# Optimization experiments

Measured on AMD Instinct MI355X. Metric: run time of the kernel, lower is better.

Reference implementation:

```python
import jax, jax.numpy as jnp
import numpy as np

N = 100000   # nodes
E = 1600000  # edges
B = 64       # graphs
F = 16       # node features
H = 128      # hidden dim
G = 8        # graph features
C = 2        # classes
NGIN = 2     # extra GIN layers after the first
BN_EPS = 1e-5


def elu01(x):
    # F.elu with alpha=0.1
    return jnp.where(x > 0, x, 0.1 * jnp.expm1(x))


def batchnorm(h, gamma, beta):
    # training-mode BatchNorm1d: biased batch statistics
    mu = h.mean(axis=0)
    var = h.var(axis=0)
    return (h - mu) * jax.lax.rsqrt(var + BN_EPS) * gamma + beta


def gin_layer(x, src, dst, W1, b1, gm, bt, W2, b2):
    # GINConv eps=0: MLP(x + sum_{j->i} x_j), then ELU(0.1)
    agg = jax.ops.segment_sum(x[src], dst, num_segments=x.shape[0])
    h = (x + agg) @ W1 + b1
    h = jax.nn.relu(batchnorm(h, gm, bt))
    return elu01(h @ W2 + b2)


def setup_inputs() -> dict:
    key = jax.random.key(0)
    ks = jax.random.split(key, 24)
    s = 0.05
    inp = {
        "h0": jax.random.normal(ks[0], (N, F), jnp.float32),
        "coord0": jax.random.normal(ks[1], (N, 3), jnp.float32),
        "g0": jax.random.normal(ks[2], (B, G), jnp.float32),
        "edge_index": jax.random.randint(ks[3], (2, E), 0, N, jnp.int32),
        "batch": jnp.sort(jax.random.randint(ks[4], (N,), 0, B, jnp.int32)),
        # first GIN layer: (F+3) -> H -> H
        "w1_0": jax.random.normal(ks[5], (F + 3, H), jnp.float32) * s,
        "b1_0": jnp.zeros((H,), jnp.float32),
        "gm_0": jnp.ones((H,), jnp.float32),
        "bt_0": jnp.zeros((H,), jnp.float32),
        "w2_0": jax.random.normal(ks[6], (H, H), jnp.float32) * s,
        "b2_0": jnp.zeros((H,), jnp.float32),
        # NGIN stacked layers: H -> H -> H
        "w1_r": jax.random.normal(ks[7], (NGIN, H, H), jnp.float32) * s,
        "b1_r": jnp.zeros((NGIN, H), jnp.float32),
        "gm_r": jnp.ones((NGIN, H), jnp.float32),
        "bt_r": jnp.zeros((NGIN, H), jnp.float32),
        "w2_r": jax.random.normal(ks[8], (NGIN, H, H), jnp.float32) * s,
        "b2_r": jnp.zeros((NGIN, H), jnp.float32),
        # classifier: (2H+G) -> H -> C
        "cw1": jax.random.normal(ks[9], (2 * H + G, H), jnp.float32) * s,
        "cb1": jnp.zeros((H,), jnp.float32),
        "cgm": jnp.ones((H,), jnp.float32),
        "cbt": jnp.zeros((H,), jnp.float32),
        "cw2": jax.random.normal(ks[10], (H, C), jnp.float32) * s,
        "cb2": jnp.zeros((C,), jnp.float32),
    }
    return inp


def reference(h0, coord0, g0, edge_index, batch,
              w1_0, b1_0, gm_0, bt_0, w2_0, b2_0,
              w1_r, b1_r, gm_r, bt_r, w2_r, b2_r,
              cw1, cb1, cgm, cbt, cw2, cb2):
    src, dst = edge_index[0], edge_index[1]
    x = jnp.concatenate([h0, coord0], axis=1)  # [N, F+3]
    x = gin_layer(x, src, dst, w1_0, b1_0, gm_0, bt_0, w2_0, b2_0)
    for i in range(NGIN):
        x = gin_layer(x, src, dst, w1_r[i], b1_r[i], gm_r[i], bt_r[i], w2_r[i], b2_r[i])
    # global mean + max pooling per graph
    nb = g0.shape[0]
    cnt = jax.ops.segment_sum(jnp.ones((x.shape[0], 1), x.dtype), batch, num_segments=nb)
    mean_p = jax.ops.segment_sum(x, batch, num_segments=nb) / jnp.maximum(cnt, 1.0)
    max_p = jax.ops.segment_max(x, batch, num_segments=nb)
    pooled = jnp.concatenate([mean_p, max_p], axis=-1)  # [B, 2H]
    z = jnp.concatenate([pooled, g0], axis=1)           # [B, 2H+G]
    z = elu01(z @ cw1 + cb1)
    z = batchnorm(z, cgm, cbt)
    logits = z @ cw2 + cb2
    return jax.nn.softmax(logits, axis=1)
```

## Files before the change

kernel.cpp:

```cpp
#include <hip/hip_runtime.h>
#include <math.h>

#define NN 100000
#define EE 1600000
#define BB 64
#define FF 16
#define HH 128
#define GG 8
#define K0 19
#define BN_EPS 1e-5f
#define PCH 16
#define BSHIFT 8
#define BNODES 256
#define NBINS 391
#define BCAP 8192
#define ACH 2048
#define NB_WP 320
#define NB_X0 12500
#define STSLOT 8

typedef short bf16x8 __attribute__((ext_vector_type(8)));
typedef float f32x4 __attribute__((ext_vector_type(4)));

__device__ __forceinline__ float elu01f(float v) {
    return v > 0.f ? v : 0.1f * (__expf(v) - 1.f);
}

__device__ __forceinline__ unsigned f2bfu(float f) {
    unsigned u = __float_as_uint(f);
    unsigned r = u + 0x7FFFu + ((u >> 16) & 1u);
    return r >> 16;
}
__device__ __forceinline__ short f2bf(float f) { return (short)f2bfu(f); }
__device__ __forceinline__ float bfu2f(unsigned short b) {
    return __uint_as_float(((unsigned)b) << 16);
}
__device__ __forceinline__ float bflo(unsigned u) { return __uint_as_float(u << 16); }
__device__ __forceinline__ float bfhi(unsigned u) { return __uint_as_float(u & 0xffff0000u); }

__global__ __launch_bounds__(256) void k_binA(const int* __restrict__ esrc, const int* __restrict__ edst,
                                              int* __restrict__ bincnt, uint2* __restrict__ binbuf) {
    __shared__ int hist[NBINS];
    __shared__ int gbase[NBINS];
    __shared__ int cur[NBINS];
    __shared__ int sc[512];
    __shared__ uint2 ebuf[ACH];
    __shared__ uint2 sorted[ACH];
    int tid = threadIdx.x;
    int e0 = blockIdx.x * ACH;
    int n = min(ACH, EE - e0);
    for (int i = tid; i < NBINS; i += 256) hist[i] = 0;
    __syncthreads();
    for (int i = tid; i < n; i += 256) {
        int s = esrc[e0 + i];
        int d = edst[e0 + i];
        ebuf[i] = make_uint2((unsigned)s, (unsigned)d);
        atomicAdd(&hist[d >> BSHIFT], 1);
    }
    __syncthreads();
    sc[tid] = (tid < NBINS) ? hist[tid] : 0;
    sc[tid + 256] = (tid + 256 < NBINS) ? hist[tid + 256] : 0;
    __syncthreads();
    for (int off = 1; off < 512; off <<= 1) {
        int a0 = sc[tid], a1 = sc[tid + 256];
        int b0 = (tid >= off) ? sc[tid - off] : 0;
        int b1 = (tid + 256 >= off) ? sc[tid + 256 - off] : 0;
        __syncthreads();
        sc[tid] = a0 + b0;
        sc[tid + 256] = a1 + b1;
        __syncthreads();
    }
    for (int b = tid; b < NBINS; b += 256) {
        int c = hist[b];
        gbase[b] = (c > 0) ? atomicAdd(&bincnt[b], c) : 0;
        cur[b] = (b > 0) ? sc[b - 1] : 0;
    }
    __syncthreads();
    for (int i = tid; i < n; i += 256) {
        uint2 e = ebuf[i];
        int b = (int)(e.y >> BSHIFT);
        int pos = atomicAdd(&cur[b], 1);
        sorted[pos] = e;
    }
    __syncthreads();
    for (int i = tid; i < n; i += 256) {
        uint2 e = sorted[i];
        int b = (int)(e.y >> BSHIFT);
        int ls = (b > 0) ? sc[b - 1] : 0;
        int gpos = gbase[b] + (i - ls);
        binbuf[(size_t)b * BCAP + gpos] = e;
    }
}

__global__ void k_binscan(const int* __restrict__ bincnt, int* __restrict__ binstart, int* __restrict__ rp,
                          const int* __restrict__ batch, int* __restrict__ gptr) {
    __shared__ int sc[512];
    int t = threadIdx.x;
    sc[t] = (t < NBINS) ? bincnt[t] : 0;
    __syncthreads();
    for (int off = 1; off < 512; off <<= 1) {
        int v = (t >= off) ? sc[t - off] : 0;
        __syncthreads();
        sc[t] += v;
        __syncthreads();
    }
    if (t < NBINS) binstart[t] = (t > 0) ? sc[t - 1] : 0;
    if (t == 0) rp[NN] = EE;
    if (t <= BB) {
        int lo = 0, hi = NN;
        while (lo < hi) { int mid = (lo + hi) >> 1; if (batch[mid] < t) lo = mid + 1; else hi = mid; }
        gptr[t] = lo;
    }
}

__global__ __launch_bounds__(256) void k_binB(const uint2* __restrict__ binbuf, const int* __restrict__ bincnt,
                                              const int* __restrict__ binstart,
                                              int* __restrict__ rp, int* __restrict__ srcs) {
    __shared__ int hist[BNODES];
    __shared__ int scx[BNODES];
    __shared__ int scur[BNODES];
    __shared__ int sbuf[BCAP];
    int b = blockIdx.x;
    int n = bincnt[b];
    int tid = threadIdx.x;
    hist[tid] = 0;
    __syncthreads();
    const uint2* eb = binbuf + (size_t)b * BCAP;
    for (int i = tid; i < n; i += 256)
        atomicAdd(&hist[eb[i].y & (BNODES - 1)], 1);
    __syncthreads();
    scx[tid] = hist[tid];
    __syncthreads();
    for (int off = 1; off < 256; off <<= 1) {
        int v = (tid >= off) ? scx[tid - off] : 0;
        __syncthreads();
        scx[tid] += v;
        __syncthreads();
    }
    int base = binstart[b];
    int excl = (tid > 0) ? scx[tid - 1] : 0;
    int node = (b << BSHIFT) + tid;
    if (node < NN) rp[node] = base + excl;
    scur[tid] = excl;
    __syncthreads();
    for (int i = tid; i < n; i += 256) {
        uint2 e = eb[i];
        int pos = atomicAdd(&scur[e.y & (BNODES - 1)], 1);
        sbuf[pos] = (int)e.x;
    }
    __syncthreads();
    for (int i = tid; i < n; i += 256) srcs[base + i] = sbuf[i];
}

__global__ __launch_bounds__(256) void k_prep(const float* __restrict__ w2_0, const float* __restrict__ w1_r,
                                              const float* __restrict__ w2_r, short* __restrict__ wt,
                                              const float* __restrict__ h0, const float* __restrict__ coord,
                                              unsigned short* __restrict__ x0) {
    int b = blockIdx.x;
    if (b < NB_WP) {
        int t = b * 256 + threadIdx.x;
        if (t >= 5 * HH * HH) return;
        int m = t >> 14;
        int rem = t & 16383;
        int col = rem >> 7;
        int k = rem & 127;
        const float* src = (m == 0) ? w2_0 : (m <= 2 ? w1_r + (size_t)(m - 1) * HH * HH
                                                     : w2_r + (size_t)(m - 3) * HH * HH);
        wt[t] = f2bf(src[k * HH + col]);
    } else {
        int i = (b - NB_WP) * 256 + threadIdx.x;
        if (i >= NN * 32) return;
        int node = i >> 5, k = i & 31;
        float v = 0.f;
        if (k < FF) v = h0[node * FF + k];
        else if (k < K0) v = coord[node * 3 + (k - FF)];
        x0[i] = (unsigned short)f2bfu(v);
    }
}

template<int K>
__global__ __launch_bounds__(256) void k_l0(const uint4* __restrict__ x4, const int* __restrict__ rp,
        const int* __restrict__ srcs, const float* __restrict__ W, const float* __restrict__ bias,
        unsigned short* __restrict__ out, float* __restrict__ gstat) {
    constexpr int SK = ((K + 3) / 4) * 4 + 4;
    __shared__ __align__(16) float yt[32 * SK];
    __shared__ float red[256];
    int tid = threadIdx.x;
    int row0 = blockIdx.x * 32;
    int wave = tid >> 6, lane = tid & 63;
    int e = lane >> 2, q = lane & 3;
    for (int rr = 0; rr < 8; ++rr) {
        int r = (wave << 3) + rr;
        int grow = row0 + r;
        float acc[8];
        if (e == 0) {
            uint4 u = x4[(size_t)grow * 4 + q];
            acc[0] = bflo(u.x); acc[1] = bfhi(u.x);
            acc[2] = bflo(u.y); acc[3] = bfhi(u.y);
            acc[4] = bflo(u.z); acc[5] = bfhi(u.z);
            acc[6] = bflo(u.w); acc[7] = bfhi(u.w);
        } else {
            #pragma unroll
            for (int j = 0; j < 8; j++) acc[j] = 0.f;
        }
        int beg = rp[grow], end = rp[grow + 1];
        for (int p = beg; p < end; p += 16) {
            bool act = e < (end - p);
            int sn = act ? srcs[p + e] : 0;
            uint4 u = x4[(size_t)sn * 4 + q];
            float m = act ? 1.f : 0.f;
            acc[0] = fmaf(m, bflo(u.x), acc[0]); acc[1] = fmaf(m, bfhi(u.x), acc[1]);
            acc[2] = fmaf(m, bflo(u.y), acc[2]); acc[3] = fmaf(m, bfhi(u.y), acc[3]);
            acc[4] = fmaf(m, bflo(u.z), acc[4]); acc[5] = fmaf(m, bfhi(u.z), acc[5]);
            acc[6] = fmaf(m, bflo(u.w), acc[6]); acc[7] = fmaf(m, bfhi(u.w), acc[7]);
        }
        #pragma unroll
        for (int mask = 4; mask <= 32; mask <<= 1)
            #pragma unroll
            for (int j = 0; j < 8; j++) acc[j] += __shfl_xor(acc[j], mask, 64);
        if (e == 0 && q < 3) {
            #pragma unroll
            for (int j = 0; j < 8; j++) yt[r * SK + q * 8 + j] = acc[j];
        }
    }
    __syncthreads();
    int col = tid & 127;
    int rg = tid >> 7;
    float facc[16];
    #pragma unroll
    for (int r = 0; r < 16; r++) facc[r] = 0.f;
    const float* ybase = &yt[rg * 16 * SK];
    int kk = 0;
    for (; kk + 4 <= K; kk += 4) {
        float w0 = W[(kk + 0) * HH + col];
        float w1 = W[(kk + 1) * HH + col];
        float w2 = W[(kk + 2) * HH + col];
        float w3 = W[(kk + 3) * HH + col];
        #pragma unroll
        for (int r = 0; r < 16; r++) {
            const float4 v = *(const float4*)&ybase[r * SK + kk];
            facc[r] = fmaf(v.x, w0, facc[r]);
            facc[r] = fmaf(v.y, w1, facc[r]);
            facc[r] = fmaf(v.z, w2, facc[r]);
            facc[r] = fmaf(v.w, w3, facc[r]);
        }
    }
    if constexpr (K % 4 != 0) {
        float w[4];
        #pragma unroll
        for (int j = 0; j < 4; j++) w[j] = (kk + j < K) ? W[(kk + j) * HH + col] : 0.f;
        #pragma unroll
        for (int r = 0; r < 16; r++) {
            const float4 v = *(const float4*)&ybase[r * SK + kk];
            facc[r] = fmaf(v.x, w[0], facc[r]);
            facc[r] = fmaf(v.y, w[1], facc[r]);
            facc[r] = fmaf(v.z, w[2], facc[r]);
            facc[r] = fmaf(v.w, w[3], facc[r]);
        }
    }
    float bcol = bias[col];
    float s = 0.f, s2 = 0.f;
    #pragma unroll
    for (int r = 0; r < 16; r++) {
        float hv = facc[r] + bcol;
        out[(size_t)(row0 + rg * 16 + r) * HH + col] = (unsigned short)f2bfu(hv);
        s += hv; s2 = fmaf(hv, hv, s2);
    }
    int sl = (blockIdx.x & (STSLOT - 1)) << 8;
    red[tid] = s; __syncthreads();
    if (tid < 128) atomicAdd(&gstat[sl + tid], s + red[tid + 128]);
    __syncthreads();
    red[tid] = s2; __syncthreads();
    if (tid < 128) atomicAdd(&gstat[sl + 128 + tid], s2 + red[tid + 128]);
}

__global__ __launch_bounds__(256) void k_agg128_bf(const unsigned* __restrict__ x, const int* __restrict__ rp,
                                                   const int* __restrict__ srcs, unsigned* __restrict__ y) {
    int w = (blockIdx.x * 256 + threadIdx.x) >> 6;
    int lane = threadIdx.x & 63;
    if (w >= NN) return;
    int beg = rp[w], end = rp[w + 1];
    unsigned us = x[(size_t)w * 64 + lane];
    float ax = bflo(us), ay = bfhi(us);
    float bx = 0.f, by = 0.f;
    float cx = 0.f, cy = 0.f;
    float dx = 0.f, dy = 0.f;
    int p = beg;
    for (; p + 16 <= end; p += 16) {
        int s0 = srcs[p + 0], s1 = srcs[p + 1], s2 = srcs[p + 2], s3 = srcs[p + 3];
        int s4 = srcs[p + 4], s5 = srcs[p + 5], s6 = srcs[p + 6], s7 = srcs[p + 7];
        int s8 = srcs[p + 8], s9 = srcs[p + 9], sa = srcs[p + 10], sb = srcs[p + 11];
        int sc_ = srcs[p + 12], sd = srcs[p + 13], se = srcs[p + 14], sf = srcs[p + 15];
        unsigned u0 = x[(size_t)s0 * 64 + lane];
        unsigned u1 = x[(size_t)s1 * 64 + lane];
        unsigned u2 = x[(size_t)s2 * 64 + lane];
        unsigned u3 = x[(size_t)s3 * 64 + lane];
        unsigned u4 = x[(size_t)s4 * 64 + lane];
        unsigned u5 = x[(size_t)s5 * 64 + lane];
        unsigned u6 = x[(size_t)s6 * 64 + lane];
        unsigned u7 = x[(size_t)s7 * 64 + lane];
        unsigned u8 = x[(size_t)s8 * 64 + lane];
        unsigned u9 = x[(size_t)s9 * 64 + lane];
        unsigned ua = x[(size_t)sa * 64 + lane];
        unsigned ub = x[(size_t)sb * 64 + lane];
        unsigned uc = x[(size_t)sc_ * 64 + lane];
        unsigned ud = x[(size_t)sd * 64 + lane];
        unsigned ue = x[(size_t)se * 64 + lane];
        unsigned uf = x[(size_t)sf * 64 + lane];
        ax += (bflo(u0) + bflo(u1)) + (bflo(u2) + bflo(u3));
        ay += (bfhi(u0) + bfhi(u1)) + (bfhi(u2) + bfhi(u3));
        bx += (bflo(u4) + bflo(u5)) + (bflo(u6) + bflo(u7));
        by += (bfhi(u4) + bfhi(u5)) + (bfhi(u6) + bfhi(u7));
        cx += (bflo(u8) + bflo(u9)) + (bflo(ua) + bflo(ub));
        cy += (bfhi(u8) + bfhi(u9)) + (bfhi(ua) + bfhi(ub));
        dx += (bflo(uc) + bflo(ud)) + (bflo(ue) + bflo(uf));
        dy += (bfhi(uc) + bfhi(ud)) + (bfhi(ue) + bfhi(uf));
    }
    for (; p + 8 <= end; p += 8) {
        int s0 = srcs[p + 0], s1 = srcs[p + 1], s2 = srcs[p + 2], s3 = srcs[p + 3];
        int s4 = srcs[p + 4], s5 = srcs[p + 5], s6 = srcs[p + 6], s7 = srcs[p + 7];
        unsigned u0 = x[(size_t)s0 * 64 + lane];
        unsigned u1 = x[(size_t)s1 * 64 + lane];
        unsigned u2 = x[(size_t)s2 * 64 + lane];
        unsigned u3 = x[(size_t)s3 * 64 + lane];
        unsigned u4 = x[(size_t)s4 * 64 + lane];
        unsigned u5 = x[(size_t)s5 * 64 + lane];
        unsigned u6 = x[(size_t)s6 * 64 + lane];
        unsigned u7 = x[(size_t)s7 * 64 + lane];
        ax += (bflo(u0) + bflo(u1)) + (bflo(u2) + bflo(u3));
        ay += (bfhi(u0) + bfhi(u1)) + (bfhi(u2) + bfhi(u3));
        bx += (bflo(u4) + bflo(u5)) + (bflo(u6) + bflo(u7));
        by += (bfhi(u4) + bfhi(u5)) + (bfhi(u6) + bfhi(u7));
    }
    for (; p < end; ++p) {
        unsigned u = x[(size_t)srcs[p] * 64 + lane];
        ax += bflo(u);
        ay += bfhi(u);
    }
    ax += bx + cx + dx;
    ay += by + cy + dy;
    y[(size_t)w * 64 + lane] = f2bfu(ax) | (f2bfu(ay) << 16);
}

__global__ __launch_bounds__(256) void k_gemm_s1(const unsigned short* __restrict__ in,
        const short* __restrict__ WT, const float* __restrict__ bias,
        unsigned short* __restrict__ out, float* __restrict__ gstat) {
    __shared__ __align__(16) short Al[64 * 136];
    __shared__ float lsum[HH], lsq[HH];
    int tid = threadIdx.x;
    if (tid < HH) { lsum[tid] = 0.f; lsq[tid] = 0.f; }
    int row0 = blockIdx.x * 64;
    {
        int r = tid >> 2;
        int k0 = (tid & 3) * 32;
        int grow = row0 + r;
        uint4* d4 = (uint4*)&Al[r * 136 + k0];
        if (grow < NN) {
            const uint4* s4 = (const uint4*)(in + (size_t)grow * HH + k0);
            d4[0] = s4[0]; d4[1] = s4[1]; d4[2] = s4[2]; d4[3] = s4[3];
        } else {
            uint4 z = {0, 0, 0, 0};
            d4[0] = z; d4[1] = z; d4[2] = z; d4[3] = z;
        }
    }
    __syncthreads();
    int wave = tid >> 6;
    int lane = tid & 63;
    int ln = lane & 15, quad = lane >> 4;
    int wcol0 = wave * 32;
    f32x4 acc[4][2];
    #pragma unroll
    for (int rt = 0; rt < 4; rt++)
        #pragma unroll
        for (int ct = 0; ct < 2; ct++) acc[rt][ct] = (f32x4){0.f, 0.f, 0.f, 0.f};
    #pragma unroll
    for (int ks = 0; ks < 4; ks++) {
        bf16x8 a[4], b[2];
        #pragma unroll
        for (int ct = 0; ct < 2; ct++)
            b[ct] = *(const bf16x8*)(WT + (size_t)(wcol0 + ct * 16 + ln) * HH + ks * 32 + quad * 8);
        #pragma unroll
        for (int rt = 0; rt < 4; rt++)
            a[rt] = *(const bf16x8*)(&Al[(rt * 16 + ln) * 136 + ks * 32 + quad * 8]);
        #pragma unroll
        for (int rt = 0; rt < 4; rt++)
            #pragma unroll
            for (int ct = 0; ct < 2; ct++)
                acc[rt][ct] = __builtin_amdgcn_mfma_f32_16x16x32_bf16(a[rt], b[ct], acc[rt][ct], 0, 0, 0);
    }
    float b0 = bias[wcol0 + ln];
    float b1 = bias[wcol0 + 16 + ln];
    float s[2] = {0.f, 0.f}, s2[2] = {0.f, 0.f};
    #pragma unroll
    for (int rt = 0; rt < 4; rt++) {
        #pragma unroll
        for (int r = 0; r < 4; r++) {
            int grow = row0 + rt * 16 + quad * 4 + r;
            if (grow < NN) {
                float hv0 = acc[rt][0][r] + b0;
                float hv1 = acc[rt][1][r] + b1;
                out[(size_t)grow * HH + wcol0 + ln] = (unsigned short)f2bfu(hv0);
                out[(size_t)grow * HH + wcol0 + 16 + ln] = (unsigned short)f2bfu(hv1);
                s[0] += hv0; s2[0] = fmaf(hv0, hv0, s2[0]);
                s[1] += hv1; s2[1] = fmaf(hv1, hv1, s2[1]);
            }
        }
    }
    atomicAdd(&lsum[wcol0 + ln], s[0]);
    atomicAdd(&lsum[wcol0 + 16 + ln], s[1]);
    atomicAdd(&lsq[wcol0 + ln], s2[0]);
    atomicAdd(&lsq[wcol0 + 16 + ln], s2[1]);
    __syncthreads();
    if (tid < HH) {
        int sl = (blockIdx.x & (STSLOT - 1)) << 8;
        atomicAdd(&gstat[sl + tid], lsum[tid]);
        atomicAdd(&gstat[sl + 128 + tid], lsq[tid]);
    }
}

__global__ __launch_bounds__(256) void k_gemm_bn(const unsigned short* __restrict__ in,
        const short* __restrict__ WT, const float* __restrict__ bias,
        const float* __restrict__ gstat, const float* __restrict__ gm, const float* __restrict__ bt,
        unsigned short* __restrict__ out) {
    __shared__ __align__(16) short Al[64 * 136];
    __shared__ __align__(16) float bnsc[HH], bnsh[HH];
    int tid = threadIdx.x;
    if (tid < HH) {
        float s = 0.f, s2 = 0.f;
        #pragma unroll
        for (int k = 0; k < STSLOT; ++k) {
            s += gstat[(k << 8) + tid];
            s2 += gstat[(k << 8) + 128 + tid];
        }
        float mu = s * (1.f / NN);
        float var = fmaxf(s2 * (1.f / NN) - mu * mu, 0.f);
        float a = gm[tid] * rsqrtf(var + BN_EPS);
        bnsc[tid] = a;
        bnsh[tid] = fmaf(-mu, a, bt[tid]);
    }
    __syncthreads();
    int row0 = blockIdx.x * 64;
    {
        int r = tid >> 2;
        int k0 = (tid & 3) * 32;
        int grow = row0 + r;
        short* dst = &Al[r * 136 + k0];
        if (grow < NN) {
            const uint4* s4 = (const uint4*)(in + (size_t)grow * HH + k0);
            unsigned* d = (unsigned*)dst;
            #pragma unroll
            for (int q = 0; q < 4; q++) {
                uint4 u = s4[q];
                float4 sc0 = *(const float4*)(bnsc + k0 + q * 8);
                float4 sh0 = *(const float4*)(bnsh + k0 + q * 8);
                float4 sc1 = *(const float4*)(bnsc + k0 + q * 8 + 4);
                float4 sh1 = *(const float4*)(bnsh + k0 + q * 8 + 4);
                float a0 = bflo(u.x), a1 = bfhi(u.x);
                float a2 = bflo(u.y), a3 = bfhi(u.y);
                float a4 = bflo(u.z), a5 = bfhi(u.z);
                float a6 = bflo(u.w), a7 = bfhi(u.w);
                a0 = fmaxf(fmaf(a0, sc0.x, sh0.x), 0.f);
                a1 = fmaxf(fmaf(a1, sc0.y, sh0.y), 0.f);
                a2 = fmaxf(fmaf(a2, sc0.z, sh0.z), 0.f);
                a3 = fmaxf(fmaf(a3, sc0.w, sh0.w), 0.f);
                a4 = fmaxf(fmaf(a4, sc1.x, sh1.x), 0.f);
                a5 = fmaxf(fmaf(a5, sc1.y, sh1.y), 0.f);
                a6 = fmaxf(fmaf(a6, sc1.z, sh1.z), 0.f);
                a7 = fmaxf(fmaf(a7, sc1.w, sh1.w), 0.f);
                d[q * 4 + 0] = f2bfu(a0) | (f2bfu(a1) << 16);
                d[q * 4 + 1] = f2bfu(a2) | (f2bfu(a3) << 16);
                d[q * 4 + 2] = f2bfu(a4) | (f2bfu(a5) << 16);
                d[q * 4 + 3] = f2bfu(a6) | (f2bfu(a7) << 16);
            }
        } else {
            uint4 z = {0, 0, 0, 0};
            uint4* d4 = (uint4*)dst;
            d4[0] = z; d4[1] = z; d4[2] = z; d4[3] = z;
        }
    }
    __syncthreads();
    int wave = tid >> 6;
    int lane = tid & 63;
    int ln = lane & 15, quad = lane >> 4;
    int wcol0 = wave * 32;
    f32x4 acc[4][2];
    #pragma unroll
    for (int rt = 0; rt < 4; rt++)
        #pragma unroll
        for (int ct = 0; ct < 2; ct++) acc[rt][ct] = (f32x4){0.f, 0.f, 0.f, 0.f};
    #pragma unroll
    for (int ks = 0; ks < 4; ks++) {
        bf16x8 a[4], b[2];
        #pragma unroll
        for (int ct = 0; ct < 2; ct++)
            b[ct] = *(const bf16x8*)(WT + (size_t)(wcol0 + ct * 16 + ln) * HH + ks * 32 + quad * 8);
        #pragma unroll
        for (int rt = 0; rt < 4; rt++)
            a[rt] = *(const bf16x8*)(&Al[(rt * 16 + ln) * 136 + ks * 32 + quad * 8]);
        #pragma unroll
        for (int rt = 0; rt < 4; rt++)
            #pragma unroll
            for (int ct = 0; ct < 2; ct++)
                acc[rt][ct] = __builtin_amdgcn_mfma_f32_16x16x32_bf16(a[rt], b[ct], acc[rt][ct], 0, 0, 0);
    }
    float b0 = bias[wcol0 + ln];
    float b1 = bias[wcol0 + 16 + ln];
    #pragma unroll
    for (int rt = 0; rt < 4; rt++) {
        #pragma unroll
        for (int r = 0; r < 4; r++) {
            int grow = row0 + rt * 16 + quad * 4 + r;
            if (grow < NN) {
                float hv0 = elu01f(acc[rt][0][r] + b0);
                float hv1 = elu01f(acc[rt][1][r] + b1);
                out[(size_t)grow * HH + wcol0 + ln] = (unsigned short)f2bfu(hv0);
                out[(size_t)grow * HH + wcol0 + 16 + ln] = (unsigned short)f2bfu(hv1);
            }
        }
    }
}

__global__ __launch_bounds__(128) void k_pool_part(const unsigned short* __restrict__ x,
                                                   const int* __restrict__ gptr,
                                                   float* __restrict__ psum, float* __restrict__ pmax) {
    int g = blockIdx.x >> 4;
    int ch = blockIdx.x & 15;
    int s = gptr[g], e = gptr[g + 1];
    int len = e - s;
    int per = (len + PCH - 1) / PCH;
    int lo = s + ch * per;
    int hi = min(lo + per, e);
    int c = threadIdx.x;
    float sm = 0.f, mx = -INFINITY;
    for (int i = lo; i < hi; ++i) {
        float v = bfu2f(x[(size_t)i * HH + c]);
        sm += v; mx = fmaxf(mx, v);
    }
    psum[(size_t)blockIdx.x * HH + c] = sm;
    pmax[(size_t)blockIdx.x * HH + c] = mx;
}

__global__ __launch_bounds__(128) void k_pool_cls1(const float* __restrict__ psum, const float* __restrict__ pmax,
                                                   const int* __restrict__ gptr, const float* __restrict__ g0,
                                                   const float* __restrict__ cw1, const float* __restrict__ cb1,
                                                   float* __restrict__ z1) {
    __shared__ float zr[264];
    int g = blockIdx.x, c = threadIdx.x;
    float sm = 0.f, mx = -INFINITY;
    for (int ch = 0; ch < PCH; ++ch) {
        sm += psum[(size_t)(g * PCH + ch) * HH + c];
        mx = fmaxf(mx, pmax[(size_t)(g * PCH + ch) * HH + c]);
    }
    int cntn = gptr[g + 1] - gptr[g];
    zr[c] = sm / (float)max(cntn, 1);
    zr[128 + c] = mx;
    if (c < GG) zr[256 + c] = g0[g * GG + c];
    __syncthreads();
    float acc = cb1[c];
    for (int k = 0; k < 264; ++k) acc = fmaf(zr[k], cw1[k * HH + c], acc);
    z1[g * HH + c] = elu01f(acc);
}

__global__ __launch_bounds__(128) void k_cls2(const float* __restrict__ z1, const float* __restrict__ cgm,
                                              const float* __restrict__ cbt, const float* __restrict__ cw2,
                                              const float* __restrict__ cb2, float* __restrict__ outp) {
    __shared__ float zn[HH * 65];
    int c = threadIdx.x;
    float s = 0.f, s2 = 0.f;
    for (int g = 0; g < BB; ++g) {
        float v = z1[g * HH + c];
        s += v; s2 = fmaf(v, v, s2);
    }
    float mu = s * (1.f / BB);
    float var = fmaxf(s2 * (1.f / BB) - mu * mu, 0.f);
    float a = cgm[c] * rsqrtf(var + BN_EPS);
    float sh = fmaf(-mu, a, cbt[c]);
    for (int g = 0; g < BB; ++g) zn[c * 65 + g] = fmaf(z1[g * HH + c], a, sh);
    __syncthreads();
    if (c < BB) {
        float l0 = cb2[0], l1 = cb2[1];
        for (int k = 0; k < HH; ++k) {
            float v = zn[k * 65 + c];
            l0 = fmaf(v, cw2[k * 2 + 0], l0);
            l1 = fmaf(v, cw2[k * 2 + 1], l1);
        }
        float m = fmaxf(l0, l1);
        float e0 = __expf(l0 - m), e1 = __expf(l1 - m);
        float inv = 1.f / (e0 + e1);
        outp[c * 2 + 0] = e0 * inv;
        outp[c * 2 + 1] = e1 * inv;
    }
}

extern "C" void kernel_launch(void* const* d_in, const int* in_sizes, int n_in,
                              void* d_out, int out_size, void* d_ws, size_t ws_size,
                              hipStream_t stream) {
    (void)in_sizes; (void)n_in; (void)out_size; (void)ws_size;
    const float* h0     = (const float*)d_in[0];
    const float* coord0 = (const float*)d_in[1];
    const float* g0     = (const float*)d_in[2];
    const int*   eidx   = (const int*)d_in[3];
    const int*   batch  = (const int*)d_in[4];
    const float* w1_0   = (const float*)d_in[5];
    const float* b1_0   = (const float*)d_in[6];
    const float* gm_0   = (const float*)d_in[7];
    const float* bt_0   = (const float*)d_in[8];
    const float* w2_0   = (const float*)d_in[9];
    const float* b2_0   = (const float*)d_in[10];
    const float* w1_r   = (const float*)d_in[11];
    const float* b1_r   = (const float*)d_in[12];
    const float* gm_r   = (const float*)d_in[13];
    const float* bt_r   = (const float*)d_in[14];
    const float* w2_r   = (const float*)d_in[15];
    const float* b2_r   = (const float*)d_in[16];
    const float* cw1    = (const float*)d_in[17];
    const float* cb1    = (const float*)d_in[18];
    const float* cgm    = (const float*)d_in[19];
    const float* cbt    = (const float*)d_in[20];
    const float* cw2    = (const float*)d_in[21];
    const float* cb2    = (const float*)d_in[22];
    float* outp = (float*)d_out;

    const int* esrc = eidx;
    const int* edst = eidx + EE;

    char* p = (char*)d_ws;
    auto alloc = [&](size_t bytes) { void* r = (void*)p; p += (bytes + 255) & ~(size_t)255; return r; };
    int*            bincnt   = (int*)alloc((size_t)NBINS * 4);
    float*          gstat    = (float*)alloc((size_t)3 * STSLOT * 256 * 4);
    unsigned short* x0bf     = (unsigned short*)alloc((size_t)NN * 32 * 2);
    unsigned short* hbf      = (unsigned short*)alloc((size_t)NN * HH * 2);
    unsigned*       xbf      = (unsigned*)alloc((size_t)NN * 64 * 4);
    unsigned*       ybf      = (unsigned*)alloc((size_t)NN * 64 * 4);
    int*            rp       = (int*)alloc((size_t)(NN + 1) * 4);
    int*            srcs     = (int*)alloc((size_t)EE * 4);
    int*            binstart = (int*)alloc((size_t)NBINS * 4);
    int*            gptr     = (int*)alloc((BB + 1) * 4);
    short*          wt       = (short*)alloc((size_t)5 * HH * HH * 2);
    float*          psum     = (float*)alloc((size_t)BB * PCH * HH * 4);
    float*          pmax     = (float*)alloc((size_t)BB * PCH * HH * 4);
    float*          z1b      = (float*)alloc((size_t)BB * HH * 4);
    uint2*          binbuf   = (uint2*)alloc((size_t)NBINS * BCAP * 8);

    const int NB_A = (EE + ACH - 1) / ACH;
    const int NB_AGG = (NN * 64 + 255) / 256;
    const int NB_G32 = NN / 32;
    const int NB_G64 = (NN + 63) / 64;

    size_t zlen = (size_t)((char*)x0bf - (char*)bincnt);
    hipMemsetAsync(bincnt, 0, zlen, stream);

    k_binA<<<NB_A, 256, 0, stream>>>(esrc, edst, bincnt, binbuf);
    k_binscan<<<1, 512, 0, stream>>>(bincnt, binstart, rp, batch, gptr);
    k_binB<<<NBINS, 256, 0, stream>>>(binbuf, bincnt, binstart, rp, srcs);
    k_prep<<<NB_WP + NB_X0, 256, 0, stream>>>(w2_0, w1_r, w2_r, wt, h0, coord0, x0bf);

    k_l0<K0><<<NB_G32, 256, 0, stream>>>((const uint4*)x0bf, rp, srcs, w1_0, b1_0, hbf, gstat);
    k_gemm_bn<<<NB_G64, 256, 0, stream>>>(hbf, wt, b2_0, gstat, gm_0, bt_0, (unsigned short*)xbf);

    for (int i = 0; i < 2; ++i) {
        float* gs = gstat + (size_t)(1 + i) * STSLOT * 256;
        k_agg128_bf<<<NB_AGG, 256, 0, stream>>>(xbf, rp, srcs, ybf);
        k_gemm_s1<<<NB_G64, 256, 0, stream>>>((const unsigned short*)ybf,
                wt + (size_t)(1 + i) * HH * HH, b1_r + i * HH, hbf, gs);
        k_gemm_bn<<<NB_G64, 256, 0, stream>>>(hbf, wt + (size_t)(3 + i) * HH * HH, b2_r + i * HH,
                                              gs, gm_r + i * HH, bt_r + i * HH, (unsigned short*)xbf);
    }

    k_pool_part<<<BB * PCH, 128, 0, stream>>>((const unsigned short*)xbf, gptr, psum, pmax);
    k_pool_cls1<<<BB, 128, 0, stream>>>(psum, pmax, gptr, g0, cw1, cb1, z1b);
    k_cls2<<<1, 128, 0, stream>>>(z1b, cgm, cbt, cw2, cb2, outp);
}
```

Baseline: 532.9 us.

## Split layer-0 gather from GEMM and fold bin scan into binB

Drops the single-block bin-scan kernel. Each binB block now computes its own base offset by reducing the counts of earlier bins, and the graph-pointer binary search moves into k_prep. The fused layer-0 aggregate+GEMM kernel, which had each wave handle 8 rows serially, is split into a one-wave-per-node gather kernel writing fp32 to a new buffer, followed by a small GEMM kernel. This raises parallelism and latency hiding in the gather, at the cost of an extra kernel launch and an fp32 intermediate round trip through memory.

```diff
diff --git a/kernel.cpp b/kernel.cpp
--- a/kernel.cpp
+++ b/kernel.cpp
@@ -92,39 +92,27 @@
     }
 }
 
-__global__ void k_binscan(const int* __restrict__ bincnt, int* __restrict__ binstart, int* __restrict__ rp,
-                          const int* __restrict__ batch, int* __restrict__ gptr) {
-    __shared__ int sc[512];
-    int t = threadIdx.x;
-    sc[t] = (t < NBINS) ? bincnt[t] : 0;
-    __syncthreads();
-    for (int off = 1; off < 512; off <<= 1) {
-        int v = (t >= off) ? sc[t - off] : 0;
-        __syncthreads();
-        sc[t] += v;
-        __syncthreads();
-    }
-    if (t < NBINS) binstart[t] = (t > 0) ? sc[t - 1] : 0;
-    if (t == 0) rp[NN] = EE;
-    if (t <= BB) {
-        int lo = 0, hi = NN;
-        while (lo < hi) { int mid = (lo + hi) >> 1; if (batch[mid] < t) lo = mid + 1; else hi = mid; }
-        gptr[t] = lo;
-    }
-}
-
 __global__ __launch_bounds__(256) void k_binB(const uint2* __restrict__ binbuf, const int* __restrict__ bincnt,
-                                              const int* __restrict__ binstart,
                                               int* __restrict__ rp, int* __restrict__ srcs) {
     __shared__ int hist[BNODES];
     __shared__ int scx[BNODES];
     __shared__ int scur[BNODES];
+    __shared__ int rsum[BNODES];
     __shared__ int sbuf[BCAP];
     int b = blockIdx.x;
     int n = bincnt[b];
     int tid = threadIdx.x;
+    int v = 0;
+    if (tid < b) v = bincnt[tid];
+    if (tid + 256 < b) v += bincnt[tid + 256];
+    rsum[tid] = v;
     hist[tid] = 0;
     __syncthreads();
+    for (int off = 128; off > 0; off >>= 1) {
+        if (tid < off) rsum[tid] += rsum[tid + off];
+        __syncthreads();
+    }
+    int base = rsum[0];
     const uint2* eb = binbuf + (size_t)b * BCAP;
     for (int i = tid; i < n; i += 256)
         atomicAdd(&hist[eb[i].y & (BNODES - 1)], 1);
@@ -132,15 +120,15 @@
     scx[tid] = hist[tid];
     __syncthreads();
     for (int off = 1; off < 256; off <<= 1) {
-        int v = (tid >= off) ? scx[tid - off] : 0;
+        int vv = (tid >= off) ? scx[tid - off] : 0;
         __syncthreads();
-        scx[tid] += v;
+        scx[tid] += vv;
         __syncthreads();
     }
-    int base = binstart[b];
     int excl = (tid > 0) ? scx[tid - 1] : 0;
     int node = (b << BSHIFT) + tid;
     if (node < NN) rp[node] = base + excl;
+    if (b == NBINS - 1 && tid == 0) rp[NN] = EE;
     scur[tid] = excl;
     __syncthreads();
     for (int i = tid; i < n; i += 256) {
@@ -155,10 +143,18 @@
 __global__ __launch_bounds__(256) void k_prep(const float* __restrict__ w2_0, const float* __restrict__ w1_r,
                                               const float* __restrict__ w2_r, short* __restrict__ wt,
                                               const float* __restrict__ h0, const float* __restrict__ coord,
-                                              unsigned short* __restrict__ x0) {
+                                              unsigned short* __restrict__ x0,
+                                              const int* __restrict__ batch, int* __restrict__ gptr) {
     int b = blockIdx.x;
+    int tid = threadIdx.x;
+    if (b == 0 && tid <= BB) {
+        int t = tid;
+        int lo = 0, hi = NN;
+        while (lo < hi) { int mid = (lo + hi) >> 1; if (batch[mid] < t) lo = mid + 1; else hi = mid; }
+        gptr[t] = lo;
+    }
     if (b < NB_WP) {
-        int t = b * 256 + threadIdx.x;
+        int t = b * 256 + tid;
         if (t >= 5 * HH * HH) return;
         int m = t >> 14;
         int rem = t & 16383;
@@ -168,7 +164,7 @@
                                                      : w2_r + (size_t)(m - 3) * HH * HH);
         wt[t] = f2bf(src[k * HH + col]);
     } else {
-        int i = (b - NB_WP) * 256 + threadIdx.x;
+        int i = (b - NB_WP) * 256 + tid;
         if (i >= NN * 32) return;
         int node = i >> 5, k = i & 31;
         float v = 0.f;
@@ -178,23 +174,17 @@
     }
 }
 
-template<int K>
-__global__ __launch_bounds__(256) void k_l0(const uint4* __restrict__ x4, const int* __restrict__ rp,
-        const int* __restrict__ srcs, const float* __restrict__ W, const float* __restrict__ bias,
-        unsigned short* __restrict__ out, float* __restrict__ gstat) {
-    constexpr int SK = ((K + 3) / 4) * 4 + 4;
-    __shared__ __align__(16) float yt[32 * SK];
-    __shared__ float red[256];
-    int tid = threadIdx.x;
-    int row0 = blockIdx.x * 32;
-    int wave = tid >> 6, lane = tid & 63;
+__global__ __launch_bounds__(256) void k_agg_small(const uint4* __restrict__ x, const int* __restrict__ rp,
+                                                   const int* __restrict__ srcs, float* __restrict__ y) {
+    int w = (blockIdx.x * 256 + threadIdx.x) >> 6;
+    int lane = threadIdx.x & 63;
+    if (w >= NN) return;
     int e = lane >> 2, q = lane & 3;
-    for (int rr = 0; rr < 8; ++rr) {
-        int r = (wave << 3) + rr;
-        int grow = row0 + r;
-        float acc[8];
+    int beg = rp[w], end = rp[w + 1];
+    float acc[8];
+    {
         if (e == 0) {
-            uint4 u = x4[(size_t)grow * 4 + q];
+            uint4 u = x[(size_t)w * 4 + q];
             acc[0] = bflo(u.x); acc[1] = bfhi(u.x);
             acc[2] = bflo(u.y); acc[3] = bfhi(u.y);
             acc[4] = bflo(u.z); acc[5] = bfhi(u.z);
@@ -203,32 +193,51 @@
             #pragma unroll
             for (int j = 0; j < 8; j++) acc[j] = 0.f;
         }
-        int beg = rp[grow], end = rp[grow + 1];
-        for (int p = beg; p < end; p += 16) {
-            bool act = e < (end - p);
-            int sn = act ? srcs[p + e] : 0;
-            uint4 u = x4[(size_t)sn * 4 + q];
-            float m = act ? 1.f : 0.f;
-            acc[0] = fmaf(m, bflo(u.x), acc[0]); acc[1] = fmaf(m, bfhi(u.x), acc[1]);
-            acc[2] = fmaf(m, bflo(u.y), acc[2]); acc[3] = fmaf(m, bfhi(u.y), acc[3]);
-            acc[4] = fmaf(m, bflo(u.z), acc[4]); acc[5] = fmaf(m, bfhi(u.z), acc[5]);
-            acc[6] = fmaf(m, bflo(u.w), acc[6]); acc[7] = fmaf(m, bfhi(u.w), acc[7]);
-        }
-        #pragma unroll
-        for (int mask = 4; mask <= 32; mask <<= 1)
-            #pragma unroll
-            for (int j = 0; j < 8; j++) acc[j] += __shfl_xor(acc[j], mask, 64);
-        if (e == 0 && q < 3) {
-            #pragma unroll
-            for (int j = 0; j < 8; j++) yt[r * SK + q * 8 + j] = acc[j];
-        }
+    }
+    for (int p = beg; p < end; p += 16) {
+        int rem = end - p;
+        bool act = e < rem;
+        int sn = act ? srcs[p + e] : 0;
+        uint4 u = x[(size_t)sn * 4 + q];
+        float m = act ? 1.f : 0.f;
+        acc[0] = fmaf(m, bflo(u.x), acc[0]); acc[1] = fmaf(m, bfhi(u.x), acc[1]);
+        acc[2] = fmaf(m, bflo(u.y), acc[2]); acc[3] = fmaf(m, bfhi(u.y), acc[3]);
+        acc[4] = fmaf(m, bflo(u.z), acc[4]); acc[5] = fmaf(m, bfhi(u.z), acc[5]);
+        acc[6] = fmaf(m, bflo(u.w), acc[6]); acc[7] = fmaf(m, bfhi(u.w), acc[7]);
+    }
+    #pragma unroll
+    for (int mask = 4; mask <= 32; mask <<= 1)
+        #pragma unroll
+        for (int j = 0; j < 8; j++)
+            acc[j] += __shfl_xor(acc[j], mask, 64);
+    if (e == 0) {
+        float4* yo = (float4*)(y + (size_t)w * 32 + q * 8);
+        yo[0] = make_float4(acc[0], acc[1], acc[2], acc[3]);
+        yo[1] = make_float4(acc[4], acc[5], acc[6], acc[7]);
+    }
+}
+
+template<int K>
+__global__ __launch_bounds__(256) void k_gemm_small(const float* __restrict__ in,
+        const float* __restrict__ W, const float* __restrict__ bias,
+        unsigned short* __restrict__ out, float* __restrict__ gstat) {
+    constexpr int SK = ((K + 3) / 4) * 4 + 4;
+    __shared__ __align__(16) float yt[32 * SK];
+    __shared__ float red[256];
+    int tid = threadIdx.x;
+    int row0 = blockIdx.x * 32;
+    for (int t = tid; t < 32 * SK; t += 256) {
+        int r = t / SK, k = t - r * SK;
+        float v = 0.f;
+        if (k < K) v = in[(size_t)(row0 + r) * 32 + k];
+        yt[t] = v;
     }
     __syncthreads();
     int col = tid & 127;
     int rg = tid >> 7;
-    float facc[16];
-    #pragma unroll
-    for (int r = 0; r < 16; r++) facc[r] = 0.f;
+    float acc[16];
+    #pragma unroll
+    for (int r = 0; r < 16; r++) acc[r] = 0.f;
     const float* ybase = &yt[rg * 16 * SK];
     int kk = 0;
     for (; kk + 4 <= K; kk += 4) {
@@ -239,10 +248,10 @@
         #pragma unroll
         for (int r = 0; r < 16; r++) {
             const float4 v = *(const float4*)&ybase[r * SK + kk];
-            facc[r] = fmaf(v.x, w0, facc[r]);
-            facc[r] = fmaf(v.y, w1, facc[r]);
-            facc[r] = fmaf(v.z, w2, facc[r]);
-            facc[r] = fmaf(v.w, w3, facc[r]);
+            acc[r] = fmaf(v.x, w0, acc[r]);
+            acc[r] = fmaf(v.y, w1, acc[r]);
+            acc[r] = fmaf(v.z, w2, acc[r]);
+            acc[r] = fmaf(v.w, w3, acc[r]);
         }
     }
     if constexpr (K % 4 != 0) {
@@ -252,17 +261,17 @@
         #pragma unroll
         for (int r = 0; r < 16; r++) {
             const float4 v = *(const float4*)&ybase[r * SK + kk];
-            facc[r] = fmaf(v.x, w[0], facc[r]);
-            facc[r] = fmaf(v.y, w[1], facc[r]);
-            facc[r] = fmaf(v.z, w[2], facc[r]);
-            facc[r] = fmaf(v.w, w[3], facc[r]);
+            acc[r] = fmaf(v.x, w[0], acc[r]);
+            acc[r] = fmaf(v.y, w[1], acc[r]);
+            acc[r] = fmaf(v.z, w[2], acc[r]);
+            acc[r] = fmaf(v.w, w[3], acc[r]);
         }
     }
     float bcol = bias[col];
     float s = 0.f, s2 = 0.f;
     #pragma unroll
     for (int r = 0; r < 16; r++) {
-        float hv = facc[r] + bcol;
+        float hv = acc[r] + bcol;
         out[(size_t)(row0 + rg * 16 + r) * HH + col] = (unsigned short)f2bfu(hv);
         s += hv; s2 = fmaf(hv, hv, s2);
     }
@@ -629,12 +638,12 @@
     int*            bincnt   = (int*)alloc((size_t)NBINS * 4);
     float*          gstat    = (float*)alloc((size_t)3 * STSLOT * 256 * 4);
     unsigned short* x0bf     = (unsigned short*)alloc((size_t)NN * 32 * 2);
+    float*          y19f     = (float*)alloc((size_t)NN * 32 * 4);
     unsigned short* hbf      = (unsigned short*)alloc((size_t)NN * HH * 2);
     unsigned*       xbf      = (unsigned*)alloc((size_t)NN * 64 * 4);
     unsigned*       ybf      = (unsigned*)alloc((size_t)NN * 64 * 4);
     int*            rp       = (int*)alloc((size_t)(NN + 1) * 4);
     int*            srcs     = (int*)alloc((size_t)EE * 4);
-    int*            binstart = (int*)alloc((size_t)NBINS * 4);
     int*            gptr     = (int*)alloc((BB + 1) * 4);
     short*          wt       = (short*)alloc((size_t)5 * HH * HH * 2);
     float*          psum     = (float*)alloc((size_t)BB * PCH * HH * 4);
@@ -651,11 +660,11 @@
     hipMemsetAsync(bincnt, 0, zlen, stream);
 
     k_binA<<<NB_A, 256, 0, stream>>>(esrc, edst, bincnt, binbuf);
-    k_binscan<<<1, 512, 0, stream>>>(bincnt, binstart, rp, batch, gptr);
-    k_binB<<<NBINS, 256, 0, stream>>>(binbuf, bincnt, binstart, rp, srcs);
-    k_prep<<<NB_WP + NB_X0, 256, 0, stream>>>(w2_0, w1_r, w2_r, wt, h0, coord0, x0bf);
-
-    k_l0<K0><<<NB_G32, 256, 0, stream>>>((const uint4*)x0bf, rp, srcs, w1_0, b1_0, hbf, gstat);
+    k_binB<<<NBINS, 256, 0, stream>>>(binbuf, bincnt, rp, srcs);
+    k_prep<<<NB_WP + NB_X0, 256, 0, stream>>>(w2_0, w1_r, w2_r, wt, h0, coord0, x0bf, batch, gptr);
+
+    k_agg_small<<<NB_AGG, 256, 0, stream>>>((const uint4*)x0bf, rp, srcs, y19f);
+    k_gemm_small<K0><<<NB_G32, 256, 0, stream>>>(y19f, w1_0, b1_0, hbf, gstat);
     k_gemm_bn<<<NB_G64, 256, 0, stream>>>(hbf, wt, b2_0, gstat, gm_0, bt_0, (unsigned short*)xbf);
 
     for (int i = 0; i < 2; ++i) {
```

Result: faster. 509.6 us (-4.4%).
